# Kernel optimization log

Measured on AMD Instinct MI355X. Metric: run time of the kernel, lower is better.

Reference implementation:

```python
import jax, jax.numpy as jnp
import numpy as np

EPS = 1e-5  # torch nn.LayerNorm default


def layer_norm(x, g, b):
    mu = jnp.mean(x, axis=-1, keepdims=True)
    var = jnp.mean(jnp.square(x - mu), axis=-1, keepdims=True)
    return (x - mu) * jax.lax.rsqrt(var + EPS) * g + b


def run_dir(g_ih_seq, w_hh, g_hh, b_hh, g_ho, b_ho, reverse):
    """Run one LayerNormLSTMCell direction over precomputed LN(x @ W_ih^T).
    g_ih_seq: [S, B, 4H]. Returns final hidden [B, H]."""
    S, B, G = g_ih_seq.shape
    H = G // 4

    def step(carry, gih_t):
        h, c = carry
        gates = gih_t + layer_norm(h @ w_hh.T, g_hh, b_hh)  # [B, 4H]
        i, f, o = jnp.split(jax.nn.sigmoid(gates[:, : 3 * H]), 3, axis=1)
        g = jnp.tanh(gates[:, 3 * H :])
        c = f * c + i * g
        h = o * jnp.tanh(layer_norm(c, g_ho, b_ho))
        return (h, c), None

    z = jnp.zeros((B, H), g_ih_seq.dtype)
    (hT, _), _ = jax.lax.scan(step, (z, z), g_ih_seq, reverse=reverse)
    return hT


def lnlstm(x, w_ih0, w_hh0, ln_ih0_g, ln_ih0_b, ln_hh0_g, ln_hh0_b, ln_ho0_g,
           ln_ho0_b, w_ih1, w_hh1, ln_ih1_g, ln_ih1_b, ln_hh1_g, ln_hh1_b,
           ln_ho1_g, ln_ho1_b):
    # x: [B, S, E] -> permute(1,0,2)
    x_seq = jnp.transpose(x, (1, 0, 2))  # [S, B, E]
    S, B, _ = x_seq.shape

    # ---- layer 0 (time-varying input) ----
    g0f = layer_norm(jnp.einsum('sbe,ge->sbg', x_seq, w_ih0[0]), ln_ih0_g[0], ln_ih0_b[0])
    hf = run_dir(g0f, w_hh0[0], ln_hh0_g[0], ln_hh0_b[0], ln_ho0_g[0], ln_ho0_b[0], False)
    g0b = layer_norm(jnp.einsum('sbe,ge->sbg', x_seq, w_ih0[1]), ln_ih0_g[1], ln_ih0_b[1])
    hb = run_dir(g0b, w_hh0[1], ln_hh0_g[1], ln_hh0_b[1], ln_ho0_g[1], ln_ho0_b[1], True)

    # Due to the `[[None]*N]*seq_len` aliasing bug in the original torch code,
    # the next layer's input is the SAME vector at every timestep:
    xc = jnp.concatenate([hf, hb], axis=1)  # [B, 2H]

    # ---- layer 1 (constant input; LN(x@W_ih^T) computed once, broadcast over time) ----
    g1f = layer_norm(xc @ w_ih1[0].T, ln_ih1_g[0], ln_ih1_b[0])
    hf1 = run_dir(jnp.broadcast_to(g1f, (S,) + g1f.shape), w_hh1[0],
                  ln_hh1_g[0], ln_hh1_b[0], ln_ho1_g[0], ln_ho1_b[0], False)
    g1b = layer_norm(xc @ w_ih1[1].T, ln_ih1_g[1], ln_ih1_b[1])
    hb1 = run_dir(jnp.broadcast_to(g1b, (S,) + g1b.shape), w_hh1[1],
                  ln_hh1_g[1], ln_hh1_b[1], ln_ho1_g[1], ln_ho1_b[1], True)

    # y = max over time of identical vectors == the vector itself
    return jnp.concatenate([hf1, hb1], axis=1)  # [B, 2H]


def setup_inputs() -> dict:
    key = jax.random.key(0)
    ks = jax.random.split(key, 20)
    B, S, E, H = 64, 48, 512, 512
    f = jnp.float32
    n = jax.random.normal
    u = jax.random.uniform
    return {
        'x': n(ks[0], (B, S, E), f),
        'text_length': jax.random.randint(ks[1], (B,), 1, S),
        'w_ih0': n(ks[2], (2, 4 * H, E), f) * 0.05,
        'w_hh0': n(ks[3], (2, 4 * H, H), f) * 0.05,
        'ln_ih0_g': u(ks[4], (2, 4 * H), f, 0.5, 1.5),
        'ln_ih0_b': n(ks[5], (2, 4 * H), f) * 0.02,
        'ln_hh0_g': u(ks[6], (2, 4 * H), f, 0.5, 1.5),
        'ln_hh0_b': n(ks[7], (2, 4 * H), f) * 0.02,
        'ln_ho0_g': u(ks[8], (2, H), f, 0.5, 1.5),
        'ln_ho0_b': n(ks[9], (2, H), f) * 0.02,
        'w_ih1': n(ks[10], (2, 4 * H, 2 * H), f) * 0.05,
        'w_hh1': n(ks[11], (2, 4 * H, H), f) * 0.05,
        'ln_ih1_g': u(ks[12], (2, 4 * H), f, 0.5, 1.5),
        'ln_ih1_b': n(ks[13], (2, 4 * H), f) * 0.02,
        'ln_hh1_g': u(ks[14], (2, 4 * H), f, 0.5, 1.5),
        'ln_hh1_b': n(ks[15], (2, 4 * H), f) * 0.02,
        'ln_ho1_g': u(ks[16], (2, H), f, 0.5, 1.5),
        'ln_ho1_b': n(ks[17], (2, H), f) * 0.02,
    }


def reference(x, text_length, w_ih0, w_hh0, ln_ih0_g, ln_ih0_b, ln_hh0_g,
              ln_hh0_b, ln_ho0_g, ln_ho0_b, w_ih1, w_hh1, ln_ih1_g, ln_ih1_b,
              ln_hh1_g, ln_hh1_b, ln_ho1_g, ln_ho1_b):
    # text_length is accepted but unused by the original forward
    return lnlstm(x, w_ih0, w_hh0, ln_ih0_g, ln_ih0_b, ln_hh0_g, ln_hh0_b,
                  ln_ho0_g, ln_ho0_b, w_ih1, w_hh1, ln_ih1_g, ln_ih1_b,
                  ln_hh1_g, ln_hh1_b, ln_ho1_g, ln_ho1_b)
```

## Files before the change

kernel.cpp:

```cpp
#include <hip/hip_runtime.h>
#include <math.h>

#define HH 512
#define BB 64
#define SS 48
#define EE 512
#define G4 2048
#define EPSF 1e-5f
#define AGENT __HIP_MEMORY_SCOPE_AGENT

typedef __attribute__((ext_vector_type(4))) float f32x4;

__device__ __forceinline__ float aload(const float* p) {
  return __hip_atomic_load(p, __ATOMIC_RELAXED, AGENT);
}
__device__ __forceinline__ void astore(float* p, float v) {
  __hip_atomic_store(p, v, __ATOMIC_RELAXED, AGENT);
}

__device__ __forceinline__ f32x4 ld4c(const float* p) {
  f32x4 v;
  asm volatile("global_load_dwordx4 %0, %1, off sc0 sc1\n\ts_waitcnt vmcnt(0)"
               : "=&v"(v) : "v"(p) : "memory");
  return v;
}
__device__ __forceinline__ void st4c(float* p, float a, float b, float tg) {
  f32x4 v; v.x = a; v.y = b; v.z = tg; v.w = 0.f;
  asm volatile("global_store_dwordx4 %0, %1, off sc0 sc1"
               :: "v"(p), "v"(v) : "memory");
}

__device__ __forceinline__ float fsigmoid(float x) {
  float t = __builtin_amdgcn_exp2f(x * -1.44269504088896f);
  return __builtin_amdgcn_rcpf(1.f + t);
}
__device__ __forceinline__ float ftanh(float x) {
  x = fminf(fmaxf(x, -10.f), 10.f);
  float t = __builtin_amdgcn_exp2f(x * 2.88539008177793f);
  return (t - 1.f) * __builtin_amdgcn_rcpf(t + 1.f);
}

__device__ __forceinline__ void gsync(int* c, int target) {
  __builtin_amdgcn_s_waitcnt(0);
  __syncthreads();
  if (threadIdx.x == 0) {
    __hip_atomic_fetch_add(c, 1, __ATOMIC_RELEASE, AGENT);
    int spins = 0;
    while (__hip_atomic_load(c, __ATOMIC_RELAXED, AGENT) < target) {
      __builtin_amdgcn_s_sleep(2);
      if (++spins > (1 << 21)) break;
    }
    (void)__hip_atomic_load(c, __ATOMIC_ACQUIRE, AGENT);
  }
  __syncthreads();
}

__global__ __launch_bounds__(256)
void gemm_ih0(const float* __restrict__ x, const float* __restrict__ w_ih0,
              float* __restrict__ G0) {
  __shared__ float As[16][65];
  __shared__ float Bs[16][65];
  const int m0 = blockIdx.y * 64;
  const int d  = m0 / (BB * SS);
  const float* Wm = w_ih0 + (size_t)d * G4 * EE;
  const int bn = blockIdx.x * 64;
  const int tid = threadIdx.x;
  const int lrow = tid >> 2;
  const int lkk  = (tid & 3) << 2;
  const int tx = tid & 15;
  const int ty = tid >> 4;
  int m  = m0 + lrow;
  int r  = m - d * (BB * SS);
  int b  = r / SS;
  int tl = r - b * SS;
  int s  = d ? (SS - 1 - tl) : tl;
  const float* arow = x + ((size_t)b * SS + s) * EE;

  float acc[4][4] = {};
  for (int k0 = 0; k0 < EE; k0 += 16) {
    float4 av = *(const float4*)(arow + k0 + lkk);
    float4 bv = *(const float4*)(Wm + (size_t)(bn + lrow) * EE + k0 + lkk);
    As[lkk+0][lrow] = av.x; As[lkk+1][lrow] = av.y; As[lkk+2][lrow] = av.z; As[lkk+3][lrow] = av.w;
    Bs[lkk+0][lrow] = bv.x; Bs[lkk+1][lrow] = bv.y; Bs[lkk+2][lrow] = bv.z; Bs[lkk+3][lrow] = bv.w;
    __syncthreads();
    #pragma unroll
    for (int k = 0; k < 16; ++k) {
      float a[4], bbv[4];
      #pragma unroll
      for (int i = 0; i < 4; ++i) a[i] = As[k][ty*4+i];
      #pragma unroll
      for (int j = 0; j < 4; ++j) bbv[j] = Bs[k][tx*4+j];
      #pragma unroll
      for (int i = 0; i < 4; ++i)
        #pragma unroll
        for (int j = 0; j < 4; ++j) acc[i][j] += a[i]*bbv[j];
    }
    __syncthreads();
  }
  for (int i = 0; i < 4; ++i)
    for (int j = 0; j < 4; ++j)
      G0[(size_t)(m0 + ty*4 + i) * G4 + bn + tx*4 + j] = acc[i][j];
}

__global__ __launch_bounds__(256)
void ln_rows(float* __restrict__ X, const float* __restrict__ gamma,
             const float* __restrict__ beta, int rows_per_d) {
  __shared__ float red[8];
  const int row = blockIdx.x;
  const int d = row / rows_per_d;
  float* xr = X + (size_t)row * G4;
  const float* gg = gamma + (size_t)d * G4;
  const float* bb = beta  + (size_t)d * G4;
  float s = 0.f, q = 0.f;
  float v[8];
  #pragma unroll
  for (int it = 0; it < 8; ++it) {
    float xv = xr[threadIdx.x + it*256];
    v[it] = xv; s += xv; q += xv*xv;
  }
  #pragma unroll
  for (int off = 32; off > 0; off >>= 1) { s += __shfl_down(s, off); q += __shfl_down(q, off); }
  int lane = threadIdx.x & 63, wid = threadIdx.x >> 6;
  if (lane == 0) { red[wid] = s; red[4+wid] = q; }
  __syncthreads();
  float ts = red[0]+red[1]+red[2]+red[3];
  float tq = red[4]+red[5]+red[6]+red[7];
  float mu = ts * (1.f/G4);
  float rstd = rsqrtf(tq*(1.f/G4) - mu*mu + EPSF);
  #pragma unroll
  for (int it = 0; it < 8; ++it) {
    int jc = threadIdx.x + it*256;
    xr[jc] = (v[it]-mu)*rstd*gg[jc] + bb[jc];
  }
}

__global__ __launch_bounds__(1024, 4)
void persist7(const float* __restrict__ whh, const float* __restrict__ Gbuf,
              long g_row_stride, long g_t_stride,
              const float* __restrict__ lnhg, const float* __restrict__ lnhb,
              const float* __restrict__ lnog, const float* __restrict__ lnob,
              float* cbuf, float* obuf, float* Rp4, float* Cpart,
              int* flagsB,
              float* fout, int nsteps,
              int mode1, const float* __restrict__ w_ih1,
              const float* __restrict__ xcb, float* g1pre,
              const float* __restrict__ ln_g1, const float* __restrict__ ln_b1,
              int* cnt_pre) {
  __shared__ float hlds[16][1024];
  __shared__ float part[16][8][64];
  __shared__ float redR[16][64];
  __shared__ float bcR[16][2];
  __shared__ float bcC[16][2];
  __shared__ float sred[32];

  const int bb = blockIdx.x;
  const int tid = threadIdx.x;

  if (mode1) {
    const int dp = bb & 1, nbp = bb >> 1;
    const int pb = tid >> 4, ns = tid & 15;
    const int col = nbp*16 + ns;
    const float* xrow = xcb + (size_t)pb * 1024;
    const float* wv_ = w_ih1 + ((size_t)dp*G4 + col) * 1024;
    float a = 0.f;
    for (int k = 0; k < 1024; k += 4) {
      float4 xv = *(const float4*)(xrow + k);
      float4 wv4 = *(const float4*)(wv_ + k);
      a += xv.x*wv4.x + xv.y*wv4.y + xv.z*wv4.z + xv.w*wv4.w;
    }
    astore(g1pre + ((size_t)dp*BB + pb) * G4 + col, a);
    gsync(cnt_pre + 0, 256);
    if (bb < 128) {
      const int ld = bb >> 6;
      float* xr = g1pre + (size_t)bb * G4;
      const float* gg = ln_g1 + (size_t)ld * G4;
      const float* be = ln_b1 + (size_t)ld * G4;
      float v0 = aload(xr + tid), v1 = aload(xr + tid + 1024);
      float s = v0 + v1, q = v0*v0 + v1*v1;
      #pragma unroll
      for (int off = 32; off > 0; off >>= 1) { s += __shfl_down(s, off); q += __shfl_down(q, off); }
      const int wv2 = tid >> 6;
      if ((tid & 63) == 0) { sred[wv2] = s; sred[16+wv2] = q; }
      __syncthreads();
      float ts = 0.f, tq = 0.f;
      #pragma unroll
      for (int i = 0; i < 16; ++i) { ts += sred[i]; tq += sred[16+i]; }
      float mu = ts * (1.f/G4);
      float rstd = rsqrtf(tq*(1.f/G4) - mu*mu + EPSF);
      astore(xr + tid,        (v0-mu)*rstd*gg[tid]      + be[tid]);
      astore(xr + tid + 1024, (v1-mu)*rstd*gg[tid+1024] + be[tid+1024]);
    }
    gsync(cnt_pre + 16, 256);
  }

  const int g  = bb & 7;
  const int d  = g >> 2;
  const int bq = g & 3;
  const int jb = bb >> 3;
  const int rowbase = d*BB + bq*16;
  const int ke = tid >> 6, nl = tid & 63;
  const int ncol = jb*16 + ((nl>>4) << 9) + (nl & 15);
  int* fB = flagsB + g*32;

  float wreg[32];
  {
    const float* wp = whh + ((size_t)d*G4 + ncol)*HH + (size_t)ke*32;
    #pragma unroll
    for (int i = 0; i < 32; ++i) wreg[i] = wp[i];
  }

  const int bl = tid >> 4, jl = tid & 15;
  const int rowc = rowbase + bl;
  const int jc = jb*16 + jl;
  const int scol = tid & 511, srh = tid >> 9;
  const float ogv = lnog[(size_t)d*HH + scol];
  const float obv = lnob[(size_t)d*HH + scol];
  const int row16 = tid >> 5, j32 = tid & 31;
  const int inv_g = (g_t_stride == 0);

  float* rpub4 = Rp4 + ((size_t)((rowbase + row16)*32 + jb) << 2);
  const float* rpp4 = Rp4 + ((size_t)((rowbase + row16)*32 + j32) << 2);

  float hg0=0,hg1=0,hg2=0,hg3=0, hb0=0,hb1=0,hb2=0,hb3=0;
  float cg0=0,cg1=0,cg2=0,cg3=0;
  if (tid < 256) {
    const float* lnhg_d = lnhg + (size_t)d*G4;
    const float* lnhb_d = lnhb + (size_t)d*G4;
    hg0 = lnhg_d[jc];        hb0 = lnhb_d[jc];
    hg1 = lnhg_d[HH+jc];     hb1 = lnhb_d[HH+jc];
    hg2 = lnhg_d[2*HH+jc];   hb2 = lnhb_d[2*HH+jc];
    hg3 = lnhg_d[3*HH+jc];   hb3 = lnhb_d[3*HH+jc];
    if (inv_g) {
      const float* gr = Gbuf + (size_t)rowc * g_row_stride;
      cg0 = gr[jc]; cg1 = gr[HH+jc]; cg2 = gr[2*HH+jc]; cg3 = gr[3*HH+jc];
    }
  }
  float creg = 0.f;

  for (int t = 0; t < nsteps; ++t) {
    const float ft1 = (float)(t + 1);
    float cv[8], ovv[8];
    #pragma unroll
    for (int i = 0; i < 8; ++i) {
      int row = i*2 + srh;
      cv[i]  = aload(cbuf + (size_t)(rowbase + row)*512 + scol);
      ovv[i] = aload(obuf + (size_t)(rowbase + row)*512 + scol);
    }
    if (tid < 512) {
      float s = aload(Cpart + ((size_t)(rowbase+row16)*32 + j32)*2 + 0);
      float q = aload(Cpart + ((size_t)(rowbase+row16)*32 + j32)*2 + 1);
      #pragma unroll
      for (int off = 16; off > 0; off >>= 1) { s += __shfl_down(s, off, 32); q += __shfl_down(q, off, 32); }
      if (j32 == 0) {
        float mu = s * (1.f/HH);
        bcC[row16][0] = mu;
        bcC[row16][1] = rsqrtf(q*(1.f/HH) - mu*mu + EPSF);
      }
    }
    __syncthreads();
    #pragma unroll
    for (int i = 0; i < 8; ++i) {
      int row = i*2 + srh;
      hlds[row][scol] = ovv[i] * ftanh((cv[i] - bcC[row][0]) * bcC[row][1] * ogv + obv);
    }
    __syncthreads();

    #pragma unroll
    for (int half = 0; half < 2; ++half) {
      #pragma unroll
      for (int b = 0; b < 8; ++b) {
        const float* hp = &hlds[half*8 + b][ke*32];
        float acc = 0.f;
        #pragma unroll
        for (int i4 = 0; i4 < 8; ++i4) {
          float4 h4 = *(const float4*)(hp + 4*i4);
          acc += h4.x*wreg[4*i4+0] + h4.y*wreg[4*i4+1]
               + h4.z*wreg[4*i4+2] + h4.w*wreg[4*i4+3];
        }
        part[ke][b][nl] = acc;
      }
      __syncthreads();
      if (tid < 512) {
        int b = tid >> 6, n2 = tid & 63;
        float r = 0.f;
        #pragma unroll
        for (int k16 = 0; k16 < 16; ++k16) r += part[k16][b][n2];
        redR[half*8 + b][n2] = r;
      }
      __syncthreads();
    }
    if (tid < 512) {
      float v1 = redR[row16][j32], v2 = redR[row16][j32+32];
      float s = v1 + v2, q = v1*v1 + v2*v2;
      #pragma unroll
      for (int off = 16; off > 0; off >>= 1) { s += __shfl_down(s, off, 32); q += __shfl_down(q, off, 32); }
      if (j32 == 0) st4c(rpub4, s, q, ft1);
    }
    float pg0 = cg0, pg1 = cg1, pg2 = cg2, pg3 = cg3;
    if (tid < 256 && !inv_g) {
      const float* gr = Gbuf + (size_t)rowc * g_row_stride + (size_t)t * g_t_stride;
      pg0 = gr[jc]; pg1 = gr[HH+jc]; pg2 = gr[2*HH+jc]; pg3 = gr[3*HH+jc];
    }
    if (tid < 512) {
      f32x4 rp = ld4c(rpp4);
      int spins = 0;
      while (rp.z < ft1) {
        __builtin_amdgcn_s_sleep(1);
        rp = ld4c(rpp4);
        if (++spins > (1 << 20)) break;
      }
      float s = rp.x, q = rp.y;
      #pragma unroll
      for (int off = 16; off > 0; off >>= 1) { s += __shfl_down(s, off, 32); q += __shfl_down(q, off, 32); }
      if (j32 == 0) {
        float mu = s * (1.f/G4);
        bcR[row16][0] = mu;
        bcR[row16][1] = rsqrtf(q*(1.f/G4) - mu*mu + EPSF);
      }
    }
    __syncthreads();

    if (tid < 256) {
      float mu = bcR[bl][0], rstd = bcR[bl][1];
      float gi = pg0 + (redR[bl][jl]    - mu)*rstd*hg0 + hb0;
      float gf = pg1 + (redR[bl][16+jl] - mu)*rstd*hg1 + hb1;
      float go = pg2 + (redR[bl][32+jl] - mu)*rstd*hg2 + hb2;
      float gt = pg3 + (redR[bl][48+jl] - mu)*rstd*hg3 + hb3;
      float iv = fsigmoid(gi), fv = fsigmoid(gf);
      float ov = fsigmoid(go), gv = ftanh(gt);
      creg = fv*creg + iv*gv;
      float cs = creg, cq = creg*creg;
      #pragma unroll
      for (int off = 8; off > 0; off >>= 1) { cs += __shfl_down(cs, off, 16); cq += __shfl_down(cq, off, 16); }
      if (jl == 0) {
        astore(Cpart + ((size_t)rowc*32 + jb)*2 + 0, cs);
        astore(Cpart + ((size_t)rowc*32 + jb)*2 + 1, cq);
      }
      astore(cbuf + (size_t)rowc*512 + jc, creg);
      astore(obuf + (size_t)rowc*512 + jc, ov);
    }
    __syncthreads();
    if (tid == 0) __hip_atomic_store(fB + jb, t + 1, __ATOMIC_RELAXED, AGENT);
    if (tid < 32) {
      int spins = 0;
      for (;;) {
        int v = __hip_atomic_load(fB + tid, __ATOMIC_RELAXED, AGENT);
        #pragma unroll
        for (int off = 16; off > 0; off >>= 1) v = min(v, __shfl_down(v, off, 32));
        v = __shfl(v, 0, 32);
        if (v >= t + 1) break;
        __builtin_amdgcn_s_sleep(1);
        if (++spins > (1 << 22)) break;
      }
    }
    __syncthreads();
  }

  {
    float cv[8], ovv[8];
    #pragma unroll
    for (int i = 0; i < 8; ++i) {
      int row = i*2 + srh;
      cv[i]  = aload(cbuf + (size_t)(rowbase + row)*512 + scol);
      ovv[i] = aload(obuf + (size_t)(rowbase + row)*512 + scol);
    }
    if (tid < 512) {
      float s = aload(Cpart + ((size_t)(rowbase+row16)*32 + j32)*2 + 0);
      float q = aload(Cpart + ((size_t)(rowbase+row16)*32 + j32)*2 + 1);
      #pragma unroll
      for (int off = 16; off > 0; off >>= 1) { s += __shfl_down(s, off, 32); q += __shfl_down(q, off, 32); }
      if (j32 == 0) {
        float mu = s * (1.f/HH);
        bcC[row16][0] = mu;
        bcC[row16][1] = rsqrtf(q*(1.f/HH) - mu*mu + EPSF);
      }
    }
    __syncthreads();
    if (jb == 0) {
      #pragma unroll
      for (int i = 0; i < 8; ++i) {
        int row = i*2 + srh;
        float h = ovv[i] * ftanh((cv[i] - bcC[row][0]) * bcC[row][1] * ogv + obv);
        fout[(size_t)(bq*16 + row) * 1024 + (size_t)d*512 + scol] = h;
      }
    }
  }
}

extern "C" void kernel_launch(void* const* d_in, const int* in_sizes, int n_in,
                              void* d_out, int out_size, void* d_ws, size_t ws_size,
                              hipStream_t stream) {
  const float* x        = (const float*)d_in[0];
  const float* w_ih0    = (const float*)d_in[2];
  const float* w_hh0    = (const float*)d_in[3];
  const float* ln_ih0_g = (const float*)d_in[4];
  const float* ln_ih0_b = (const float*)d_in[5];
  const float* ln_hh0_g = (const float*)d_in[6];
  const float* ln_hh0_b = (const float*)d_in[7];
  const float* ln_ho0_g = (const float*)d_in[8];
  const float* ln_ho0_b = (const float*)d_in[9];
  const float* w_ih1    = (const float*)d_in[10];
  const float* w_hh1    = (const float*)d_in[11];
  const float* ln_ih1_g = (const float*)d_in[12];
  const float* ln_ih1_b = (const float*)d_in[13];
  const float* ln_hh1_g = (const float*)d_in[14];
  const float* ln_hh1_b = (const float*)d_in[15];
  const float* ln_ho1_g = (const float*)d_in[16];
  const float* ln_ho1_b = (const float*)d_in[17];
  float* out = (float*)d_out;

  float* G0    = (float*)d_ws;
  float* g1pre = G0 + (size_t)2*BB*SS*G4;
  float* xcb   = g1pre + (size_t)2*BB*G4;
  float* Rp4   = xcb + (size_t)BB*1024;
  float* Cpart = Rp4 + (size_t)128*32*4;
  float* cbuf  = Cpart + (size_t)128*32*2;
  float* obuf  = cbuf + (size_t)128*512;
  int*   ints  = (int*)(obuf + (size_t)128*512);
  int*   fB0     = ints;
  int*   fB1     = ints + 256;
  int*   cnt_pre = ints + 512;

  const size_t zr_floats = (size_t)128*32*4 + (size_t)128*32*2 + 2*(size_t)128*512;

  hipMemsetAsync(Rp4, 0, zr_floats*sizeof(float) + 576*sizeof(int), stream);

  hipLaunchKernelGGL(gemm_ih0, dim3(G4/64, (2*BB*SS)/64), dim3(256), 0, stream,
      x, w_ih0, G0);
  hipLaunchKernelGGL(ln_rows, dim3(2*BB*SS), dim3(256), 0, stream,
      G0, ln_ih0_g, ln_ih0_b, BB*SS);

  hipLaunchKernelGGL(persist7, dim3(256), dim3(1024), 0, stream,
      w_hh0, G0, (long)SS*G4, (long)G4,
      ln_hh0_g, ln_hh0_b, ln_ho0_g, ln_ho0_b,
      cbuf, obuf, Rp4, Cpart, fB0, xcb, SS,
      0, (const float*)nullptr, (const float*)nullptr, (float*)nullptr,
      (const float*)nullptr, (const float*)nullptr, (int*)nullptr);

  hipMemsetAsync(Rp4, 0, zr_floats*sizeof(float), stream);

  hipLaunchKernelGGL(persist7, dim3(256), dim3(1024), 0, stream,
      w_hh1, g1pre, (long)G4, 0L,
      ln_hh1_g, ln_hh1_b, ln_ho1_g, ln_ho1_b,
      cbuf, obuf, Rp4, Cpart, fB1, out, SS,
      1, w_ih1, xcb, g1pre, ln_ih1_g, ln_ih1_b, cnt_pre);
}
```

Baseline: 1.963 ms.

## Replicate LSTM cell update per block via double-buffered recurrent-GEMM exchange

Restructures the persistent recurrent kernel so each block publishes its slice of h@W_hh (plus LN partial sums) to a double-buffered global buffer, then after one flag barrier every block in the group reads the full 16x2048 pre-activation tile and redundantly computes gates, cell state and LN(c) locally in LDS. This removes the second exchange per step (cell/output partials and c/o buffers) and the per-partner polling on Rp4, leaving one group barrier per timestep. In exchange, each block reads 32x more global data per step and repeats the elementwise gate and LN work, and the flag array gets padded spacing.

```diff
diff --git a/kernel.cpp b/kernel.cpp
--- a/kernel.cpp
+++ b/kernel.cpp
@@ -9,25 +9,11 @@
 #define EPSF 1e-5f
 #define AGENT __HIP_MEMORY_SCOPE_AGENT
 
-typedef __attribute__((ext_vector_type(4))) float f32x4;
-
 __device__ __forceinline__ float aload(const float* p) {
   return __hip_atomic_load(p, __ATOMIC_RELAXED, AGENT);
 }
 __device__ __forceinline__ void astore(float* p, float v) {
   __hip_atomic_store(p, v, __ATOMIC_RELAXED, AGENT);
-}
-
-__device__ __forceinline__ f32x4 ld4c(const float* p) {
-  f32x4 v;
-  asm volatile("global_load_dwordx4 %0, %1, off sc0 sc1\n\ts_waitcnt vmcnt(0)"
-               : "=&v"(v) : "v"(p) : "memory");
-  return v;
-}
-__device__ __forceinline__ void st4c(float* p, float a, float b, float tg) {
-  f32x4 v; v.x = a; v.y = b; v.z = tg; v.w = 0.f;
-  asm volatile("global_store_dwordx4 %0, %1, off sc0 sc1"
-               :: "v"(p), "v"(v) : "memory");
 }
 
 __device__ __forceinline__ float fsigmoid(float x) {
@@ -135,20 +121,20 @@
 }
 
 __global__ __launch_bounds__(1024, 4)
-void persist7(const float* __restrict__ whh, const float* __restrict__ Gbuf,
+void persistR(const float* __restrict__ whh, const float* __restrict__ Gbuf,
               long g_row_stride, long g_t_stride,
               const float* __restrict__ lnhg, const float* __restrict__ lnhb,
               const float* __restrict__ lnog, const float* __restrict__ lnob,
-              float* cbuf, float* obuf, float* Rp4, float* Cpart,
-              int* flagsB,
+              float* Rbuf, float* Rp, int* flags,
               float* fout, int nsteps,
               int mode1, const float* __restrict__ w_ih1,
               const float* __restrict__ xcb, float* g1pre,
               const float* __restrict__ ln_g1, const float* __restrict__ ln_b1,
               int* cnt_pre) {
-  __shared__ float hlds[16][1024];
+  __shared__ float hlds[16][520];
   __shared__ float part[16][8][64];
-  __shared__ float redR[16][64];
+  __shared__ float c_lds[16][512];
+  __shared__ float o_lds[16][512];
   __shared__ float bcR[16][2];
   __shared__ float bcC[16][2];
   __shared__ float sred[32];
@@ -159,16 +145,16 @@
   if (mode1) {
     const int dp = bb & 1, nbp = bb >> 1;
     const int pb = tid >> 4, ns = tid & 15;
-    const int col = nbp*16 + ns;
+    const int col1 = nbp*16 + ns;
     const float* xrow = xcb + (size_t)pb * 1024;
-    const float* wv_ = w_ih1 + ((size_t)dp*G4 + col) * 1024;
+    const float* wv_ = w_ih1 + ((size_t)dp*G4 + col1) * 1024;
     float a = 0.f;
     for (int k = 0; k < 1024; k += 4) {
       float4 xv = *(const float4*)(xrow + k);
       float4 wv4 = *(const float4*)(wv_ + k);
       a += xv.x*wv4.x + xv.y*wv4.y + xv.z*wv4.z + xv.w*wv4.w;
     }
-    astore(g1pre + ((size_t)dp*BB + pb) * G4 + col, a);
+    astore(g1pre + ((size_t)dp*BB + pb) * G4 + col1, a);
     gsync(cnt_pre + 0, 256);
     if (bb < 128) {
       const int ld = bb >> 6;
@@ -200,7 +186,7 @@
   const int rowbase = d*BB + bq*16;
   const int ke = tid >> 6, nl = tid & 63;
   const int ncol = jb*16 + ((nl>>4) << 9) + (nl & 15);
-  int* fB = flagsB + g*32;
+  int* fL = flags + g*1024;
 
   float wreg[32];
   {
@@ -209,61 +195,29 @@
     for (int i = 0; i < 32; ++i) wreg[i] = wp[i];
   }
 
-  const int bl = tid >> 4, jl = tid & 15;
-  const int rowc = rowbase + bl;
-  const int jc = jb*16 + jl;
-  const int scol = tid & 511, srh = tid >> 9;
-  const float ogv = lnog[(size_t)d*HH + scol];
-  const float obv = lnob[(size_t)d*HH + scol];
+  const int col = tid & 511, rh = tid >> 9;
   const int row16 = tid >> 5, j32 = tid & 31;
-  const int inv_g = (g_t_stride == 0);
-
-  float* rpub4 = Rp4 + ((size_t)((rowbase + row16)*32 + jb) << 2);
-  const float* rpp4 = Rp4 + ((size_t)((rowbase + row16)*32 + j32) << 2);
-
-  float hg0=0,hg1=0,hg2=0,hg3=0, hb0=0,hb1=0,hb2=0,hb3=0;
-  float cg0=0,cg1=0,cg2=0,cg3=0;
-  if (tid < 256) {
-    const float* lnhg_d = lnhg + (size_t)d*G4;
-    const float* lnhb_d = lnhb + (size_t)d*G4;
-    hg0 = lnhg_d[jc];        hb0 = lnhb_d[jc];
-    hg1 = lnhg_d[HH+jc];     hb1 = lnhb_d[HH+jc];
-    hg2 = lnhg_d[2*HH+jc];   hb2 = lnhb_d[2*HH+jc];
-    hg3 = lnhg_d[3*HH+jc];   hb3 = lnhb_d[3*HH+jc];
-    if (inv_g) {
-      const float* gr = Gbuf + (size_t)rowc * g_row_stride;
-      cg0 = gr[jc]; cg1 = gr[HH+jc]; cg2 = gr[2*HH+jc]; cg3 = gr[3*HH+jc];
-    }
-  }
-  float creg = 0.f;
+
+  const float* lnhg_d = lnhg + (size_t)d*G4;
+  const float* lnhb_d = lnhb + (size_t)d*G4;
+  const float hg0 = lnhg_d[col],        hb0 = lnhb_d[col];
+  const float hg1 = lnhg_d[HH+col],     hb1 = lnhb_d[HH+col];
+  const float hg2 = lnhg_d[2*HH+col],   hb2 = lnhb_d[2*HH+col];
+  const float hg3 = lnhg_d[3*HH+col],   hb3 = lnhb_d[3*HH+col];
+  const float ogv = lnog[(size_t)d*HH + col];
+  const float obv = lnob[(size_t)d*HH + col];
+
+  {
+    float* hz = &hlds[0][0];
+    for (int u = tid; u < 16*520; u += 1024) hz[u] = 0.f;
+    float* cz = &c_lds[0][0];
+    for (int u = tid; u < 16*512; u += 1024) cz[u] = 0.f;
+  }
+  __syncthreads();
 
   for (int t = 0; t < nsteps; ++t) {
-    const float ft1 = (float)(t + 1);
-    float cv[8], ovv[8];
-    #pragma unroll
-    for (int i = 0; i < 8; ++i) {
-      int row = i*2 + srh;
-      cv[i]  = aload(cbuf + (size_t)(rowbase + row)*512 + scol);
-      ovv[i] = aload(obuf + (size_t)(rowbase + row)*512 + scol);
-    }
-    if (tid < 512) {
-      float s = aload(Cpart + ((size_t)(rowbase+row16)*32 + j32)*2 + 0);
-      float q = aload(Cpart + ((size_t)(rowbase+row16)*32 + j32)*2 + 1);
-      #pragma unroll
-      for (int off = 16; off > 0; off >>= 1) { s += __shfl_down(s, off, 32); q += __shfl_down(q, off, 32); }
-      if (j32 == 0) {
-        float mu = s * (1.f/HH);
-        bcC[row16][0] = mu;
-        bcC[row16][1] = rsqrtf(q*(1.f/HH) - mu*mu + EPSF);
-      }
-    }
-    __syncthreads();
-    #pragma unroll
-    for (int i = 0; i < 8; ++i) {
-      int row = i*2 + srh;
-      hlds[row][scol] = ovv[i] * ftanh((cv[i] - bcC[row][0]) * bcC[row][1] * ogv + obv);
-    }
-    __syncthreads();
+    float* RbufP = Rbuf + (size_t)(t & 1) * (128*2048);
+    float* RpP   = Rp   + (size_t)(t & 1) * (128*64);
 
     #pragma unroll
     for (int half = 0; half < 2; ++half) {
@@ -285,31 +239,38 @@
         float r = 0.f;
         #pragma unroll
         for (int k16 = 0; k16 < 16; ++k16) r += part[k16][b][n2];
-        redR[half*8 + b][n2] = r;
+        int row = half*8 + b;
+        int nc2 = jb*16 + ((n2>>4) << 9) + (n2 & 15);
+        astore(RbufP + (size_t)(rowbase + row)*2048 + nc2, r);
+        float s = r, q = r*r;
+        #pragma unroll
+        for (int off = 32; off > 0; off >>= 1) { s += __shfl_down(s, off); q += __shfl_down(q, off); }
+        if (n2 == 0) {
+          astore(RpP + ((size_t)(rowbase + row)*32 + jb)*2 + 0, s);
+          astore(RpP + ((size_t)(rowbase + row)*32 + jb)*2 + 1, q);
+        }
       }
       __syncthreads();
     }
+
+    if (tid == 0) __hip_atomic_store(fL + jb*32, t + 1, __ATOMIC_RELAXED, AGENT);
+    if (tid < 32) {
+      int spins = 0;
+      for (;;) {
+        int v = __hip_atomic_load(fL + tid*32, __ATOMIC_RELAXED, AGENT);
+        #pragma unroll
+        for (int off = 16; off > 0; off >>= 1) v = min(v, __shfl_down(v, off, 32));
+        v = __shfl(v, 0, 32);
+        if (v >= t + 1) break;
+        __builtin_amdgcn_s_sleep(1);
+        if (++spins > (1 << 22)) break;
+      }
+    }
+    __syncthreads();
+
     if (tid < 512) {
-      float v1 = redR[row16][j32], v2 = redR[row16][j32+32];
-      float s = v1 + v2, q = v1*v1 + v2*v2;
-      #pragma unroll
-      for (int off = 16; off > 0; off >>= 1) { s += __shfl_down(s, off, 32); q += __shfl_down(q, off, 32); }
-      if (j32 == 0) st4c(rpub4, s, q, ft1);
-    }
-    float pg0 = cg0, pg1 = cg1, pg2 = cg2, pg3 = cg3;
-    if (tid < 256 && !inv_g) {
-      const float* gr = Gbuf + (size_t)rowc * g_row_stride + (size_t)t * g_t_stride;
-      pg0 = gr[jc]; pg1 = gr[HH+jc]; pg2 = gr[2*HH+jc]; pg3 = gr[3*HH+jc];
-    }
-    if (tid < 512) {
-      f32x4 rp = ld4c(rpp4);
-      int spins = 0;
-      while (rp.z < ft1) {
-        __builtin_amdgcn_s_sleep(1);
-        rp = ld4c(rpp4);
-        if (++spins > (1 << 20)) break;
-      }
-      float s = rp.x, q = rp.y;
+      float s = aload(RpP + ((size_t)(rowbase+row16)*32 + j32)*2 + 0);
+      float q = aload(RpP + ((size_t)(rowbase+row16)*32 + j32)*2 + 1);
       #pragma unroll
       for (int off = 16; off > 0; off >>= 1) { s += __shfl_down(s, off, 32); q += __shfl_down(q, off, 32); }
       if (j32 == 0) {
@@ -320,53 +281,38 @@
     }
     __syncthreads();
 
-    if (tid < 256) {
-      float mu = bcR[bl][0], rstd = bcR[bl][1];
-      float gi = pg0 + (redR[bl][jl]    - mu)*rstd*hg0 + hb0;
-      float gf = pg1 + (redR[bl][16+jl] - mu)*rstd*hg1 + hb1;
-      float go = pg2 + (redR[bl][32+jl] - mu)*rstd*hg2 + hb2;
-      float gt = pg3 + (redR[bl][48+jl] - mu)*rstd*hg3 + hb3;
+    float Rv[32];
+    #pragma unroll
+    for (int i = 0; i < 8; ++i) {
+      const float* Rrow = RbufP + (size_t)(rowbase + i*2 + rh)*2048 + col;
+      Rv[4*i+0] = aload(Rrow);        Rv[4*i+1] = aload(Rrow + 512);
+      Rv[4*i+2] = aload(Rrow + 1024); Rv[4*i+3] = aload(Rrow + 1536);
+    }
+    #pragma unroll
+    for (int i = 0; i < 8; ++i) {
+      const int r = i*2 + rh;
+      const float* gr = Gbuf + (size_t)(rowbase + r)*g_row_stride
+                             + (size_t)t*g_t_stride + col;
+      float mu = bcR[r][0], rstd = bcR[r][1];
+      float gi = gr[0]    + (Rv[4*i+0]-mu)*rstd*hg0 + hb0;
+      float gf = gr[512]  + (Rv[4*i+1]-mu)*rstd*hg1 + hb1;
+      float go = gr[1024] + (Rv[4*i+2]-mu)*rstd*hg2 + hb2;
+      float gt = gr[1536] + (Rv[4*i+3]-mu)*rstd*hg3 + hb3;
       float iv = fsigmoid(gi), fv = fsigmoid(gf);
       float ov = fsigmoid(go), gv = ftanh(gt);
-      creg = fv*creg + iv*gv;
-      float cs = creg, cq = creg*creg;
-      #pragma unroll
-      for (int off = 8; off > 0; off >>= 1) { cs += __shfl_down(cs, off, 16); cq += __shfl_down(cq, off, 16); }
-      if (jl == 0) {
-        astore(Cpart + ((size_t)rowc*32 + jb)*2 + 0, cs);
-        astore(Cpart + ((size_t)rowc*32 + jb)*2 + 1, cq);
-      }
-      astore(cbuf + (size_t)rowc*512 + jc, creg);
-      astore(obuf + (size_t)rowc*512 + jc, ov);
-    }
-    __syncthreads();
-    if (tid == 0) __hip_atomic_store(fB + jb, t + 1, __ATOMIC_RELAXED, AGENT);
-    if (tid < 32) {
-      int spins = 0;
-      for (;;) {
-        int v = __hip_atomic_load(fB + tid, __ATOMIC_RELAXED, AGENT);
-        #pragma unroll
-        for (int off = 16; off > 0; off >>= 1) v = min(v, __shfl_down(v, off, 32));
-        v = __shfl(v, 0, 32);
-        if (v >= t + 1) break;
-        __builtin_amdgcn_s_sleep(1);
-        if (++spins > (1 << 22)) break;
-      }
-    }
-    __syncthreads();
-  }
-
-  {
-    float cv[8], ovv[8];
-    #pragma unroll
-    for (int i = 0; i < 8; ++i) {
-      int row = i*2 + srh;
-      cv[i]  = aload(cbuf + (size_t)(rowbase + row)*512 + scol);
-      ovv[i] = aload(obuf + (size_t)(rowbase + row)*512 + scol);
-    }
+      float cn = fv * c_lds[r][col] + iv * gv;
+      c_lds[r][col] = cn;
+      o_lds[r][col] = ov;
+    }
+    __syncthreads();
+
     if (tid < 512) {
-      float s = aload(Cpart + ((size_t)(rowbase+row16)*32 + j32)*2 + 0);
-      float q = aload(Cpart + ((size_t)(rowbase+row16)*32 + j32)*2 + 1);
+      float s = 0.f, q = 0.f;
+      #pragma unroll
+      for (int i = 0; i < 16; ++i) {
+        float cvv = c_lds[row16][j32 + 32*i];
+        s += cvv; q += cvv*cvv;
+      }
       #pragma unroll
       for (int off = 16; off > 0; off >>= 1) { s += __shfl_down(s, off, 32); q += __shfl_down(q, off, 32); }
       if (j32 == 0) {
@@ -376,13 +322,21 @@
       }
     }
     __syncthreads();
-    if (jb == 0) {
-      #pragma unroll
-      for (int i = 0; i < 8; ++i) {
-        int row = i*2 + srh;
-        float h = ovv[i] * ftanh((cv[i] - bcC[row][0]) * bcC[row][1] * ogv + obv);
-        fout[(size_t)(bq*16 + row) * 1024 + (size_t)d*512 + scol] = h;
-      }
+
+    #pragma unroll
+    for (int i = 0; i < 8; ++i) {
+      const int r = i*2 + rh;
+      hlds[r][col] = o_lds[r][col]
+          * ftanh((c_lds[r][col] - bcC[r][0]) * bcC[r][1] * ogv + obv);
+    }
+    __syncthreads();
+  }
+
+  if (jb == 0) {
+    #pragma unroll
+    for (int i = 0; i < 8; ++i) {
+      const int r = i*2 + rh;
+      fout[(size_t)(bq*16 + r) * 1024 + (size_t)d*512 + col] = hlds[r][col];
     }
   }
 }
@@ -412,36 +366,30 @@
   float* G0    = (float*)d_ws;
   float* g1pre = G0 + (size_t)2*BB*SS*G4;
   float* xcb   = g1pre + (size_t)2*BB*G4;
-  float* Rp4   = xcb + (size_t)BB*1024;
-  float* Cpart = Rp4 + (size_t)128*32*4;
-  float* cbuf  = Cpart + (size_t)128*32*2;
-  float* obuf  = cbuf + (size_t)128*512;
-  int*   ints  = (int*)(obuf + (size_t)128*512);
-  int*   fB0     = ints;
-  int*   fB1     = ints + 256;
-  int*   cnt_pre = ints + 512;
-
-  const size_t zr_floats = (size_t)128*32*4 + (size_t)128*32*2 + 2*(size_t)128*512;
-
-  hipMemsetAsync(Rp4, 0, zr_floats*sizeof(float) + 576*sizeof(int), stream);
+  float* Rbuf  = xcb + (size_t)BB*1024;
+  float* Rp    = Rbuf + (size_t)2*128*2048;
+  int*   ints  = (int*)(Rp + (size_t)2*128*64);
+  int*   fL0     = ints;
+  int*   fL1     = ints + 8192;
+  int*   cnt_pre = ints + 16384;
+
+  hipMemsetAsync(ints, 0, 16448*sizeof(int), stream);
 
   hipLaunchKernelGGL(gemm_ih0, dim3(G4/64, (2*BB*SS)/64), dim3(256), 0, stream,
       x, w_ih0, G0);
   hipLaunchKernelGGL(ln_rows, dim3(2*BB*SS), dim3(256), 0, stream,
       G0, ln_ih0_g, ln_ih0_b, BB*SS);
 
-  hipLaunchKernelGGL(persist7, dim3(256), dim3(1024), 0, stream,
+  hipLaunchKernelGGL(persistR, dim3(256), dim3(1024), 0, stream,
       w_hh0, G0, (long)SS*G4, (long)G4,
       ln_hh0_g, ln_hh0_b, ln_ho0_g, ln_ho0_b,
-      cbuf, obuf, Rp4, Cpart, fB0, xcb, SS,
+      Rbuf, Rp, fL0, xcb, SS,
       0, (const float*)nullptr, (const float*)nullptr, (float*)nullptr,
       (const float*)nullptr, (const float*)nullptr, (int*)nullptr);
 
-  hipMemsetAsync(Rp4, 0, zr_floats*sizeof(float), stream);
-
-  hipLaunchKernelGGL(persist7, dim3(256), dim3(1024), 0, stream,
+  hipLaunchKernelGGL(persistR, dim3(256), dim3(1024), 0, stream,
       w_hh1, g1pre, (long)G4, 0L,
       ln_hh1_g, ln_hh1_b, ln_ho1_g, ln_ho1_b,
-      cbuf, obuf, Rp4, Cpart, fB1, out, SS,
+      Rbuf, Rp, fL1, out, SS,
       1, w_ih1, xcb, g1pre, ln_ih1_g, ln_ih1_b, cnt_pre);
 }
```

Result: slower. 2.031 ms (+3.5%).
